# Performance work log

Measured on AMD Instinct MI355X. Metric: run time of the kernel, lower is better.

## Reference

```python
import jax, jax.numpy as jnp
import numpy as np

# Module constants (match init_kwargs / torch defaults)
NUM_HEADS = 8
A, B_COEF, C_COEF = 0.5, 1.0, 1.0
EPS = 1e-12  # torch F.normalize eps


def _l2_normalize(x):
    n = jnp.maximum(jnp.linalg.norm(x, axis=-1, keepdims=True), EPS)
    return x / n


def setup_inputs() -> dict:
    key = jax.random.key(0)
    ks = jax.random.split(key, 4)
    Bb, N, C = 1, 4096, 384
    x = jax.random.normal(ks[0], (Bb, N, C), dtype=jnp.float32)
    qkv_w = jax.random.normal(ks[1], (3 * C, C), dtype=jnp.float32) * 0.02
    qkv_b = jnp.zeros((3 * C,), dtype=jnp.float32)
    proj_w = jax.random.normal(ks[2], (C, C), dtype=jnp.float32) * 0.02
    proj_b = jnp.zeros((C,), dtype=jnp.float32)
    temperature = jnp.ones((1, NUM_HEADS, 1, 1), dtype=jnp.float32)
    return {"x": x, "qkv_w": qkv_w, "qkv_b": qkv_b, "proj_w": proj_w,
            "proj_b": proj_b, "temperature": temperature}


def reference(x, qkv_w, qkv_b, proj_w, proj_b, temperature):
    Bb, N, C = x.shape
    H = NUM_HEADS
    d = C // H
    scale = d ** 0.25

    qkv = x @ qkv_w.T + qkv_b                       # (B, N, 3C)
    qkv = qkv.reshape(Bb, N, 3, H, d).transpose(2, 0, 3, 1, 4)  # (3, B, H, N, d)
    q, k, v = qkv[0], qkv[1], qkv[2]
    q = q * (C ** -0.5)

    # efficient attention (N > N0 = d^2 + d + 1)
    v1 = jnp.concatenate([jnp.ones((Bb, H, N, 1), dtype=v.dtype), v], axis=-1)  # (B,H,N,d+1)
    # normalize_input=True path
    q = _l2_normalize(q) * (scale * temperature)
    k = _l2_normalize(k) * scale
    v1 = v1 / N

    # kv_mod = box(k,k)^T @ v1  ->  (B, H, d, d, d+1)
    kv_mod = jnp.einsum('bhni,bhnj,bhnf->bhijf', k, k, v1)
    # quadratic term: a * box(q,q) @ kv_mod
    y = A * jnp.einsum('bhni,bhnj,bhijf->bhnf', q, q, kv_mod)
    # linear term: scale^2 * b * q @ (k^T @ v1)
    kv = jnp.einsum('bhnd,bhnf->bhdf', k, v1)
    y = y + (scale ** 2) * B_COEF * jnp.einsum('bhnd,bhdf->bhnf', q, kv)
    # constant term: scale^4 * c * sum_n v1
    y = y + (scale ** 4) * C_COEF * jnp.sum(v1, axis=-2, keepdims=True)

    y_norm, y_out = y[..., :1], y[..., 1:]
    out = y_out / y_norm                             # (B, H, N, d)

    out = out.transpose(0, 2, 1, 3).reshape(Bb, N, C)
    out = out @ proj_w.T + proj_b
    return out
```

## Files before the change

kernel.cpp:

```cpp
#include <hip/hip_runtime.h>

#define HN 8
#define NN 4096
#define CC 384
#define DD 48
#define DP 64
#define NPAIR 1225
#define PPAD 1280
#define MPF 52

typedef unsigned short ushort;
typedef unsigned int uint;
typedef __attribute__((ext_vector_type(8))) short short8;
typedef __attribute__((ext_vector_type(4))) float f32x4;

__device__ __forceinline__ float4 ld4(const float* p){ return *reinterpret_cast<const float4*>(p); }
__device__ __forceinline__ void st4(float* p, const float4& v){ *reinterpret_cast<float4*>(p) = v; }

#define RAW_BAR() asm volatile("s_waitcnt lgkmcnt(0)\ns_barrier" ::: "memory")

__device__ __forceinline__ uint bf16rtn(float x){
  uint u = __float_as_uint(x);
  return (u + 0x7FFFu + ((u >> 16) & 1u)) >> 16;
}

__global__ __launch_bounds__(256) void split_f32(const float* __restrict__ in,
                                                 ushort* __restrict__ hi,
                                                 ushort* __restrict__ lo,
                                                 int n4) {
  int idx = blockIdx.x * 256 + threadIdx.x;
  if (idx >= n4) return;
  float4 v = ld4(in + (size_t)idx * 4);
  float bv[4] = {v.x, v.y, v.z, v.w};
  uint hu[2], lu[2];
#pragma unroll
  for (int e = 0; e < 2; ++e) {
    float x0 = bv[2*e], x1 = bv[2*e+1];
    uint h0 = bf16rtn(x0), h1 = bf16rtn(x1);
    float d0 = x0 - __uint_as_float(h0 << 16);
    float d1 = x1 - __uint_as_float(h1 << 16);
    hu[e] = h0 | (h1 << 16);
    lu[e] = (__float_as_uint(d0) >> 16) | (__float_as_uint(d1) & 0xFFFF0000u);
  }
  *reinterpret_cast<uint2*>(hi + (size_t)idx*4) = make_uint2(hu[0], hu[1]);
  *reinterpret_cast<uint2*>(lo + (size_t)idx*4) = make_uint2(lu[0], lu[1]);
}

#define GST 40
__global__ __launch_bounds__(256) void gemm_bf16(const ushort* __restrict__ Ah,
                                                 const ushort* __restrict__ Al,
                                                 const float*  __restrict__ Bw,
                                                 const float*  __restrict__ bias,
                                                 float* __restrict__ Cm,
                                                 int M, int Nc, int K) {
  __shared__ ushort AsH[2][128*GST], AsL[2][128*GST];
  __shared__ ushort BsH[2][64*GST],  BsL[2][64*GST];
  const int tid = threadIdx.x;
  const int n0 = blockIdx.x * 64;
  const int m0 = blockIdx.y * 128;
  const int lane = tid & 63, wv = tid >> 6;
  const int wr = wv >> 1, wc = wv & 1;
  const int lr = lane & 15, lg = lane >> 4;
  const int ar = tid >> 1, ap = (tid & 1) << 4;
  const int br = tid >> 2, bp = (tid & 3) << 3;
  const ushort* gAh = Ah + (size_t)(m0 + ar) * K + ap;
  const ushort* gAl = Al + (size_t)(m0 + ar) * K + ap;
  const float*  gB  = Bw + (size_t)(n0 + br) * K + bp;
  uint4 rah0, rah1, ral0, ral1;
  float4 rb0, rb1;
#define G_LOAD(T) { int kk = (T)*32; \
    rah0 = *reinterpret_cast<const uint4*>(gAh + kk); \
    rah1 = *reinterpret_cast<const uint4*>(gAh + kk + 8); \
    ral0 = *reinterpret_cast<const uint4*>(gAl + kk); \
    ral1 = *reinterpret_cast<const uint4*>(gAl + kk + 8); \
    rb0 = ld4(gB + kk); rb1 = ld4(gB + kk + 4); }
#define G_WRITE(BUF) { \
    *reinterpret_cast<uint4*>(&AsH[BUF][ar*GST+ap])   = rah0; \
    *reinterpret_cast<uint4*>(&AsH[BUF][ar*GST+ap+8]) = rah1; \
    *reinterpret_cast<uint4*>(&AsL[BUF][ar*GST+ap])   = ral0; \
    *reinterpret_cast<uint4*>(&AsL[BUF][ar*GST+ap+8]) = ral1; \
    float bv[8] = {rb0.x,rb0.y,rb0.z,rb0.w,rb1.x,rb1.y,rb1.z,rb1.w}; \
    uint hu[4], lu[4]; \
    _Pragma("unroll") for (int e = 0; e < 4; ++e) { \
      float x0 = bv[2*e], x1 = bv[2*e+1]; \
      uint h0 = bf16rtn(x0), h1 = bf16rtn(x1); \
      float d0 = x0 - __uint_as_float(h0 << 16); \
      float d1 = x1 - __uint_as_float(h1 << 16); \
      hu[e] = h0 | (h1 << 16); \
      lu[e] = (__float_as_uint(d0) >> 16) | (__float_as_uint(d1) & 0xFFFF0000u); } \
    *reinterpret_cast<uint4*>(&BsH[BUF][br*GST+bp]) = make_uint4(hu[0],hu[1],hu[2],hu[3]); \
    *reinterpret_cast<uint4*>(&BsL[BUF][br*GST+bp]) = make_uint4(lu[0],lu[1],lu[2],lu[3]); }

  f32x4 acc[4][2];
#pragma unroll
  for (int pf = 0; pf < 4; ++pf)
#pragma unroll
    for (int ff = 0; ff < 2; ++ff) acc[pf][ff] = (f32x4)0.f;

  G_LOAD(0);
  G_WRITE(0);
  G_LOAD(1);
  const int NT = K / 32;
  int cur = 0;
  RAW_BAR();
  for (int t = 0; t < NT; ++t) {
    short8 a_h[4], a_l[4], b_h[2], b_l[2];
#pragma unroll
    for (int pf = 0; pf < 4; ++pf) {
      int row = wr*64 + pf*16 + lr;
      a_h[pf] = *reinterpret_cast<const short8*>(&AsH[cur][row*GST + lg*8]);
      a_l[pf] = *reinterpret_cast<const short8*>(&AsL[cur][row*GST + lg*8]);
    }
#pragma unroll
    for (int ff = 0; ff < 2; ++ff) {
      int col = wc*32 + ff*16 + lr;
      b_h[ff] = *reinterpret_cast<const short8*>(&BsH[cur][col*GST + lg*8]);
      b_l[ff] = *reinterpret_cast<const short8*>(&BsL[cur][col*GST + lg*8]);
    }
    if (t < NT-1) { G_WRITE(cur^1); }
    if (t < NT-2) { G_LOAD(t+2); }
#pragma unroll
    for (int pf = 0; pf < 4; ++pf)
#pragma unroll
      for (int ff = 0; ff < 2; ++ff) {
        acc[pf][ff] = __builtin_amdgcn_mfma_f32_16x16x32_bf16(a_h[pf], b_h[ff], acc[pf][ff], 0, 0, 0);
        acc[pf][ff] = __builtin_amdgcn_mfma_f32_16x16x32_bf16(a_h[pf], b_l[ff], acc[pf][ff], 0, 0, 0);
        acc[pf][ff] = __builtin_amdgcn_mfma_f32_16x16x32_bf16(a_l[pf], b_h[ff], acc[pf][ff], 0, 0, 0);
      }
    RAW_BAR();
    cur ^= 1;
  }
#pragma unroll
  for (int pf = 0; pf < 4; ++pf)
#pragma unroll
    for (int ff = 0; ff < 2; ++ff) {
      int col = n0 + wc*32 + ff*16 + lr;
      float bs = bias[col];
#pragma unroll
      for (int reg = 0; reg < 4; ++reg) {
        int row = m0 + wr*64 + pf*16 + lg*4 + reg;
        Cm[(size_t)row*Nc + col] = acc[pf][ff][reg] + bs;
      }
    }
#undef G_LOAD
#undef G_WRITE
}

__global__ __launch_bounds__(256) void prep2(const float* __restrict__ qkv,
                                             const float* __restrict__ temperature,
                                             float* __restrict__ Qb,
                                             float* __restrict__ KbT,
                                             ushort* __restrict__ VhT,
                                             ushort* __restrict__ VlT) {
  __shared__ float Ks[64*65];
  __shared__ float Vs[64*65];
  const int nb = blockIdx.x;
  const int h  = blockIdx.y;
  const int lane = threadIdx.x & 63;
  const int w = threadIdx.x >> 6;
  const float temp = temperature[h];
  const float CINV = 0.05103103630798288f;
  const float S4   = 2.6321480259049848f;
  for (int r = 0; r < 16; ++r) {
    const int nl = w*16 + r;
    const int n  = nb*64 + nl;
    const float* row = qkv + (size_t)n * (3*CC) + h * DD;
    float qv = (lane < DD) ? row[lane] : 0.f;
    float kv = (lane < DD) ? row[CC + lane] : 0.f;
    float vv = (lane >= 1 && lane <= DD) ? row[2*CC + lane - 1] : 0.f;
    float qs = qv * CINV;
    float q2 = qs * qs;
    float k2 = kv * kv;
#pragma unroll
    for (int off = 32; off > 0; off >>= 1) {
      q2 += __shfl_xor(q2, off);
      k2 += __shfl_xor(k2, off);
    }
    float qn = qs / fmaxf(sqrtf(q2), 1e-12f) * (S4 * temp);
    float kn = kv / fmaxf(sqrtf(k2), 1e-12f) * S4;
    float qo = (lane < DD) ? qn : ((lane == DD) ? 6.928203230275509f : 0.f);
    float ko = (lane < DD) ? kn : ((lane == DD) ? 1.f : 0.f);
    float vo = (lane == 0) ? (1.f/NN) : ((lane <= DD) ? vv * (1.f/NN) : 0.f);
    Qb[((size_t)h * NN + n) * DP + lane] = qo;
    Ks[nl*65 + lane] = ko;
    Vs[nl*65 + lane] = vo;
  }
  __syncthreads();
  const int ch = threadIdx.x >> 2;
  const int q4 = threadIdx.x & 3;
  float kc[16], vc[16];
#pragma unroll
  for (int e = 0; e < 16; ++e) {
    int nl = q4*16 + e;
    kc[e] = Ks[nl*65 + ch];
    vc[e] = Vs[nl*65 + ch];
  }
  size_t tbase = ((size_t)h*64 + ch) * NN + nb*64 + q4*16;
#pragma unroll
  for (int e = 0; e < 16; e += 4)
    st4(KbT + tbase + e, make_float4(kc[e], kc[e+1], kc[e+2], kc[e+3]));
  uint hu[8], lu[8];
#pragma unroll
  for (int e = 0; e < 8; ++e) {
    float v0 = vc[2*e], v1 = vc[2*e+1];
    uint h0 = bf16rtn(v0), h1 = bf16rtn(v1);
    float d0 = v0 - __uint_as_float(h0 << 16);
    float d1 = v1 - __uint_as_float(h1 << 16);
    uint t0 = __float_as_uint(d0), t1 = __float_as_uint(d1);
    hu[e] = h0 | (h1 << 16);
    lu[e] = (t0 >> 16) | (t1 & 0xFFFF0000u);
  }
  *reinterpret_cast<uint4*>(VhT + tbase)     = make_uint4(hu[0],hu[1],hu[2],hu[3]);
  *reinterpret_cast<uint4*>(VhT + tbase + 8) = make_uint4(hu[4],hu[5],hu[6],hu[7]);
  *reinterpret_cast<uint4*>(VlT + tbase)     = make_uint4(lu[0],lu[1],lu[2],lu[3]);
  *reinterpret_cast<uint4*>(VlT + tbase + 8) = make_uint4(lu[4],lu[5],lu[6],lu[7]);
}

#define KST 40
#define KNST 36
__global__ __launch_bounds__(256) void kvmod_mfma(const float* __restrict__ KbT,
                                                  const ushort* __restrict__ VhT,
                                                  const ushort* __restrict__ VlT,
                                                  float* __restrict__ Mp) {
  __shared__ ushort KKh[256*KST];
  __shared__ ushort KKl[256*KST];
  __shared__ float  KnS[64*KNST];
  __shared__ ushort VhS[64*KST];
  __shared__ ushort VlS[64*KST];
  const int tid  = threadIdx.x;
  const int bid  = blockIdx.x;
  const int h    = bid & 7;
  const int idx  = bid >> 3;
  const int p0   = (idx % 5) * 256;
  const int part = idx / 5;
  const int nbase = part * 512;
  int ii = 63, jj = 63;
  {
    int pg = p0 + tid;
    if (pg < NPAIR) {
      int i = 0, rem = pg;
      while (rem >= 49 - i) { rem -= 49 - i; ++i; }
      ii = i; jj = i + rem;
    }
  }
  const float* krow_i = &KnS[ii*KNST];
  const float* krow_j = &KnS[jj*KNST];
  const int sch = tid >> 2;
  const int sq  = tid & 3;
  const size_t kgbase = ((size_t)h*64 + sch) * NN + nbase;
  const int lane = tid & 63, wv = tid >> 6;
  const int lr = lane & 15, lg = lane >> 4;
  f32x4 acc[4][4];
#pragma unroll
  for (int a = 0; a < 4; ++a)
#pragma unroll
    for (int b = 0; b < 4; ++b) acc[a][b] = (f32x4)0.f;

  float4 pa0, pa1; uint4 pvh, pvl;
#define PRE_LOAD(T) { int k0_ = (T)*32; \
    pa0 = ld4(KbT + kgbase + k0_ + sq*8); \
    pa1 = ld4(KbT + kgbase + k0_ + sq*8 + 4); \
    pvh = *reinterpret_cast<const uint4*>(VhT + kgbase + k0_ + sq*8); \
    pvl = *reinterpret_cast<const uint4*>(VlT + kgbase + k0_ + sq*8); }
#define STAGE_WRITE() { \
    st4(&KnS[sch*KNST + sq*8], pa0); \
    st4(&KnS[sch*KNST + sq*8 + 4], pa1); \
    *reinterpret_cast<uint4*>(&VhS[sch*KST + sq*8]) = pvh; \
    *reinterpret_cast<uint4*>(&VlS[sch*KST + sq*8]) = pvl; }

  PRE_LOAD(0);
  for (int t = 0; t < 16; ++t) {
    RAW_BAR();
    STAGE_WRITE();
    if (t < 15) { PRE_LOAD(t+1); }
    RAW_BAR();
    {
      uint hu[16], lu[16];
#pragma unroll
      for (int g = 0; g < 8; ++g) {
        float4 a = ld4(krow_i + g*4);
        float4 b = ld4(krow_j + g*4);
        float m0 = a.x*b.x, m1 = a.y*b.y, m2 = a.z*b.z, m3 = a.w*b.w;
        uint h0 = bf16rtn(m0), h1 = bf16rtn(m1), h2 = bf16rtn(m2), h3 = bf16rtn(m3);
        float d0 = m0 - __uint_as_float(h0 << 16);
        float d1 = m1 - __uint_as_float(h1 << 16);
        float d2 = m2 - __uint_as_float(h2 << 16);
        float d3 = m3 - __uint_as_float(h3 << 16);
        uint t0 = __float_as_uint(d0), t1 = __float_as_uint(d1);
        uint t2 = __float_as_uint(d2), t3 = __float_as_uint(d3);
        hu[2*g]   = h0 | (h1 << 16);
        hu[2*g+1] = h2 | (h3 << 16);
        lu[2*g]   = (t0 >> 16) | (t1 & 0xFFFF0000u);
        lu[2*g+1] = (t2 >> 16) | (t3 & 0xFFFF0000u);
      }
      uint4* dh = reinterpret_cast<uint4*>(&KKh[tid*KST]);
      uint4* dl = reinterpret_cast<uint4*>(&KKl[tid*KST]);
      dh[0] = make_uint4(hu[0],hu[1],hu[2],hu[3]);
      dh[1] = make_uint4(hu[4],hu[5],hu[6],hu[7]);
      dh[2] = make_uint4(hu[8],hu[9],hu[10],hu[11]);
      dh[3] = make_uint4(hu[12],hu[13],hu[14],hu[15]);
      dl[0] = make_uint4(lu[0],lu[1],lu[2],lu[3]);
      dl[1] = make_uint4(lu[4],lu[5],lu[6],lu[7]);
      dl[2] = make_uint4(lu[8],lu[9],lu[10],lu[11]);
      dl[3] = make_uint4(lu[12],lu[13],lu[14],lu[15]);
    }
    RAW_BAR();
    short8 ah[4], al[4], bh[4], bl[4];
#pragma unroll
    for (int pf = 0; pf < 4; ++pf) {
      int prow = wv*64 + pf*16 + lr;
      ah[pf] = *reinterpret_cast<const short8*>(&KKh[prow*KST + lg*8]);
      al[pf] = *reinterpret_cast<const short8*>(&KKl[prow*KST + lg*8]);
    }
#pragma unroll
    for (int ff = 0; ff < 4; ++ff) {
      int frow = ff*16 + lr;
      bh[ff] = *reinterpret_cast<const short8*>(&VhS[frow*KST + lg*8]);
      bl[ff] = *reinterpret_cast<const short8*>(&VlS[frow*KST + lg*8]);
    }
#pragma unroll
    for (int pf = 0; pf < 4; ++pf)
#pragma unroll
      for (int ff = 0; ff < 4; ++ff) {
        acc[pf][ff] = __builtin_amdgcn_mfma_f32_16x16x32_bf16(ah[pf], bh[ff], acc[pf][ff], 0, 0, 0);
        acc[pf][ff] = __builtin_amdgcn_mfma_f32_16x16x32_bf16(ah[pf], bl[ff], acc[pf][ff], 0, 0, 0);
        acc[pf][ff] = __builtin_amdgcn_mfma_f32_16x16x32_bf16(al[pf], bh[ff], acc[pf][ff], 0, 0, 0);
      }
  }
  float* out = Mp + ((size_t)(part*HN + h) * PPAD + p0 + wv*64) * MPF;
#pragma unroll
  for (int pf = 0; pf < 4; ++pf)
#pragma unroll
    for (int ff = 0; ff < 4; ++ff) {
      int f = ff*16 + lr;
      if (f < MPF) {
#pragma unroll
        for (int reg = 0; reg < 4; ++reg) {
          int prow = pf*16 + lg*4 + reg;
          out[prow*MPF + f] = acc[pf][ff][reg];
        }
      }
    }
#undef PRE_LOAD
#undef STAGE_WRITE
}

__global__ __launch_bounds__(256) void reduce_mirror(const float* __restrict__ Mp,
                                                     ushort* __restrict__ Mbh,
                                                     ushort* __restrict__ Mbl,
                                                     float* __restrict__ Mnorm) {
  const int pb = blockIdx.x;
  const int h  = blockIdx.y;
  const int pl = threadIdx.x & 63;
  const int fq0 = threadIdx.x >> 6;
  const int p = pb*64 + pl;
  if (p >= NPAIR) return;
  int i = 0, rem = p;
  while (rem >= 49 - i) { rem -= 49 - i; ++i; }
  const int j = i + rem;
  for (int fq = fq0; fq < 13; fq += 4) {
    float4 s = make_float4(0.f, 0.f, 0.f, 0.f);
#pragma unroll
    for (int part = 0; part < 8; ++part) {
      float4 a = ld4(Mp + ((size_t)(part*HN + h) * PPAD + p) * MPF + fq*4);
      s.x += a.x; s.y += a.y; s.z += a.z; s.w += a.w;
    }
    float sv[4] = {s.x, s.y, s.z, s.w};
#pragma unroll
    for (int c = 0; c < 4; ++c) {
      int f = fq*4 + c;
      float v = sv[c];
      uint hb = bf16rtn(v);
      float d = v - __uint_as_float(hb << 16);
      ushort lb = (ushort)(__float_as_uint(d) >> 16);
      size_t a1 = (((size_t)h*49 + i)*64 + f)*64 + j;
      size_t a2 = (((size_t)h*49 + j)*64 + f)*64 + i;
      Mbh[a1] = (ushort)hb; Mbl[a1] = lb;
      Mbh[a2] = (ushort)hb; Mbl[a2] = lb;
    }
    if (p == NPAIR-1) st4(&Mnorm[h*64 + fq*4], s);
  }
}

__global__ __launch_bounds__(256, 3) void y_mfma(const float* __restrict__ Qb,
                                                 const ushort* __restrict__ Mbh,
                                                 const ushort* __restrict__ Mbl,
                                                 float* __restrict__ Yp) {
  __shared__ float QT[28*128];
  __shared__ ushort Mt[2][2][32*64];
  const int tid = threadIdx.x;
  const int bid = blockIdx.x;
  const int h   = bid & 7;
  const int rest = bid >> 3;
  const int n0  = (rest & 31) * 128;
  const int z   = rest >> 5;
  const int zi = z >> 1;
  const int zf = z & 1;
  const int ibase = zi * 25;
  const int ni = zi ? 24 : 25;
  const int lane = tid & 63;
  const int wv = tid >> 6;
  const int lr = lane & 15, lg = lane >> 4;

  {
    const int ng = (ni + 3) >> 2;
    for (int v = tid; v < ng*128; v += 256) {
      int r = v & 127;
      int cg = v >> 7;
      float4 q = ld4(Qb + ((size_t)h*NN + n0 + r)*DP + ibase + cg*4);
      QT[(cg*4+0)*128 + r] = q.x;
      QT[(cg*4+1)*128 + r] = q.y;
      QT[(cg*4+2)*128 + r] = q.z;
      QT[(cg*4+3)*128 + r] = q.w;
    }
  }
  short8 ah[2][2], al[2][2];
#pragma unroll
  for (int m = 0; m < 2; ++m) {
    const float* qr = Qb + ((size_t)h*NN + n0 + wv*32 + m*16 + lr)*DP + lg*8;
#pragma unroll
    for (int kc = 0; kc < 2; ++kc) {
      float4 v0 = ld4(qr + kc*32);
      float4 v1 = ld4(qr + kc*32 + 4);
      float qv[8] = {v0.x,v0.y,v0.z,v0.w,v1.x,v1.y,v1.z,v1.w};
      union { uint u[4]; short8 s; } chh, cll;
#pragma unroll
      for (int e = 0; e < 4; ++e) {
        float x0 = qv[2*e], x1 = qv[2*e+1];
        uint h0 = bf16rtn(x0), h1 = bf16rtn(x1);
        float d0 = x0 - __uint_as_float(h0 << 16);
        float d1 = x1 - __uint_as_float(h1 << 16);
        chh.u[e] = h0 | (h1 << 16);
        cll.u[e] = (__float_as_uint(d0) >> 16) | (__float_as_uint(d1) & 0xFFFF0000u);
      }
      ah[m][kc] = chh.s;
      al[m][kc] = cll.s;
    }
  }
  const int sp   = tid >> 7;
  const int ss   = tid & 127;
  const int srow = ss >> 2;
  const int sc2  = (ss & 3) * 2;
  const ushort* gsrc = (sp ? Mbl : Mbh) + (size_t)h*49*4096 + (zf*32 + srow)*64 + sc2*8;
  uint4 pre[2];
#define Y_LOAD(I) { const uint4* gp = reinterpret_cast<const uint4*>(gsrc + (size_t)(I)*4096); \
    pre[0] = gp[0]; pre[1] = gp[1]; }
#define Y_WRITE(BUF) { _Pragma("unroll") for (int e = 0; e < 2; ++e) { \
    int slot = (sc2 + e) ^ (srow & 7); \
    *reinterpret_cast<uint4*>(&Mt[BUF][sp][srow*64 + slot*8]) = pre[e]; } }

  Y_LOAD(ibase);
  Y_WRITE(0);
  Y_LOAD(ibase+1);

  f32x4 ya[2][2];
#pragma unroll
  for (int m = 0; m < 2; ++m)
#pragma unroll
    for (int ff = 0; ff < 2; ++ff) ya[m][ff] = (f32x4)0.f;

  int cur = 0;
  RAW_BAR();
  for (int li = 0; li < ni; ++li) {
    short8 bh[2][2], bl[2][2];
#pragma unroll
    for (int kc = 0; kc < 2; ++kc)
#pragma unroll
      for (int ff = 0; ff < 2; ++ff) {
        int row = ff*16 + lr;
        int slot = (kc*4 + lg) ^ (row & 7);
        bh[kc][ff] = *reinterpret_cast<const short8*>(&Mt[cur][0][row*64 + slot*8]);
        bl[kc][ff] = *reinterpret_cast<const short8*>(&Mt[cur][1][row*64 + slot*8]);
      }
    if (li < ni-1) { Y_WRITE(cur^1); }
    if (li < ni-2) { Y_LOAD(ibase+li+2); }
#pragma unroll
    for (int m = 0; m < 2; ++m) {
      float4 qi = ld4(&QT[li*128 + wv*32 + m*16 + lg*4]);
#pragma unroll
      for (int ff = 0; ff < 2; ++ff) {
        f32x4 acc = (f32x4)0.f;
        acc = __builtin_amdgcn_mfma_f32_16x16x32_bf16(ah[m][0], bh[0][ff], acc, 0, 0, 0);
        acc = __builtin_amdgcn_mfma_f32_16x16x32_bf16(ah[m][0], bl[0][ff], acc, 0, 0, 0);
        acc = __builtin_amdgcn_mfma_f32_16x16x32_bf16(al[m][0], bh[0][ff], acc, 0, 0, 0);
        acc = __builtin_amdgcn_mfma_f32_16x16x32_bf16(ah[m][1], bh[1][ff], acc, 0, 0, 0);
        acc = __builtin_amdgcn_mfma_f32_16x16x32_bf16(ah[m][1], bl[1][ff], acc, 0, 0, 0);
        acc = __builtin_amdgcn_mfma_f32_16x16x32_bf16(al[m][1], bh[1][ff], acc, 0, 0, 0);
        ya[m][ff][0] += qi.x * acc[0];
        ya[m][ff][1] += qi.y * acc[1];
        ya[m][ff][2] += qi.z * acc[2];
        ya[m][ff][3] += qi.w * acc[3];
      }
    }
    RAW_BAR();
    cur ^= 1;
  }
  float* out = Yp + ((size_t)(zi*HN + h) * NN) * 64;
#pragma unroll
  for (int m = 0; m < 2; ++m)
#pragma unroll
    for (int ff = 0; ff < 2; ++ff) {
      int f = zf*32 + ff*16 + lr;
#pragma unroll
      for (int reg = 0; reg < 4; ++reg) {
        int row = n0 + wv*32 + m*16 + lg*4 + reg;
        out[(size_t)row*64 + f] = ya[m][ff][reg];
      }
    }
#undef Y_LOAD
#undef Y_WRITE
}

__global__ __launch_bounds__(256) void y_combine(const float* __restrict__ Yp,
                                                 const float* __restrict__ Mnorm,
                                                 ushort* __restrict__ AttnH,
                                                 ushort* __restrict__ AttnL) {
  const int h = blockIdx.y;
  const int t = threadIdx.x;
  const int r = blockIdx.x*64 + (t >> 2);
  const int fq = t & 3;
  const int lane = t & 63;
  const float* p0 = Yp + ((size_t)h*NN + r)*64 + fq*16;
  const float* p1 = Yp + ((size_t)(HN+h)*NN + r)*64 + fq*16;
  float y[16];
#pragma unroll
  for (int g = 0; g < 4; ++g) {
    float4 a = ld4(p0 + g*4);
    float4 b = ld4(p1 + g*4);
    float4 m = ld4(Mnorm + h*64 + fq*16 + g*4);
    y[g*4+0] = 0.5f*(a.x+b.x) + 24.f*m.x;
    y[g*4+1] = 0.5f*(a.y+b.y) + 24.f*m.y;
    y[g*4+2] = 0.5f*(a.z+b.z) + 24.f*m.z;
    y[g*4+3] = 0.5f*(a.w+b.w) + 24.f*m.w;
  }
  float y0 = __shfl(y[0], lane & ~3);
  float inv = 1.f / y0;
#pragma unroll
  for (int e = 0; e < 16; ++e) {
    int f = fq*16 + e;
    if (f >= 1 && f <= DD) {
      float o = y[e] * inv;
      uint hb = bf16rtn(o);
      float d = o - __uint_as_float(hb << 16);
      size_t a = (size_t)r*CC + h*DD + (f-1);
      AttnH[a] = (ushort)hb;
      AttnL[a] = (ushort)(__float_as_uint(d) >> 16);
    }
  }
}

extern "C" void kernel_launch(void* const* d_in, const int* in_sizes, int n_in,
                              void* d_out, int out_size, void* d_ws, size_t ws_size,
                              hipStream_t stream) {
  const float* x      = (const float*)d_in[0];
  const float* qkv_w  = (const float*)d_in[1];
  const float* qkv_b  = (const float*)d_in[2];
  const float* proj_w = (const float*)d_in[3];
  const float* proj_b = (const float*)d_in[4];
  const float* temp   = (const float*)d_in[5];
  float* ws = (float*)d_ws;

  float*  qkv  = ws;
  float*  Mp   = ws;
  float*  Yp   = ws;
  float*  Qb   = ws + 4718592;
  ushort* Xh   = (ushort*)(ws + 6815744);
  ushort* Xl   = Xh + 1572864;
  float*  KbT  = ws + 6815744;
  ushort* Mbh  = (ushort*)(ws + 6815744);
  ushort* Mbl  = Mbh + 1605632;
  float*  Mnorm= ws + 6815744 + 1605632;
  ushort* VhT  = (ushort*)(ws + 8912896);
  ushort* VlT  = (ushort*)(ws + 9961472);
  ushort* AttnH= (ushort*)(ws + 8912896);
  ushort* AttnL= AttnH + 1572864;

  split_f32<<<1536, 256, 0, stream>>>(x, Xh, Xl, NN*CC/4);
  {
    dim3 g(1152/64, 4096/128);
    gemm_bf16<<<g, 256, 0, stream>>>(Xh, Xl, qkv_w, qkv_b, qkv, 4096, 1152, 384);
  }
  {
    dim3 g(64, HN);
    prep2<<<g, 256, 0, stream>>>(qkv, temp, Qb, KbT, VhT, VlT);
  }
  kvmod_mfma<<<320, 256, 0, stream>>>(KbT, VhT, VlT, Mp);
  hipMemsetAsync((void*)Mbh, 0, 2*(size_t)1605632*2 + 2048, stream);
  {
    dim3 g(PPAD/64, HN);
    reduce_mirror<<<g, 256, 0, stream>>>(Mp, Mbh, Mbl, Mnorm);
  }
  y_mfma<<<1024, 256, 0, stream>>>(Qb, Mbh, Mbl, Yp);
  {
    dim3 g(4096/64, HN);
    y_combine<<<g, 256, 0, stream>>>(Yp, Mnorm, AttnH, AttnL);
  }
  {
    dim3 g(384/64, 4096/128);
    gemm_bf16<<<g, 256, 0, stream>>>(AttnH, AttnL, proj_w, proj_b, (float*)d_out, 4096, 384, 384);
  }
}
```

Before: 201.4 us.

## Exploit pair symmetry in quadratic attention term with packed upper-triangle layout

Instead of mirroring the symmetric kv_mod tensor to a full 49x49 layout and contracting q with it in two stages, the reduction now stores only upper-triangle pairs (diagonal halved) in a chunked, transposed layout. The y kernel builds q_i*q_j products on the fly and feeds them as the MFMA A operand over the packed pair dimension. This roughly halves the K dimension and the M tensor traffic, and drops the 0.5 factor in the combine step to match. The cost is recomputing pair products and the bf16 hi/lo split per tile, plus a more intricate chunk index mapping.

```diff
diff --git a/kernel.cpp b/kernel.cpp
--- a/kernel.cpp
+++ b/kernel.cpp
@@ -8,6 +8,8 @@
 #define NPAIR 1225
 #define PPAD 1280
 #define MPF 52
+#define NP2 1792
+#define QRS 68
 
 typedef unsigned short ushort;
 typedef unsigned int uint;
@@ -22,6 +24,16 @@
 __device__ __forceinline__ uint bf16rtn(float x){
   uint u = __float_as_uint(x);
   return (u + 0x7FFFu + ((u >> 16) & 1u)) >> 16;
+}
+
+__device__ __forceinline__ void chunk_ij(int c, int& i, int& jb){
+  if (c < 56)       { i = c/7;            jb = c%7; }
+  else if (c < 104) { int t=c-56;  i = 8  + t/6; jb = 1 + t%6; }
+  else if (c < 144) { int t=c-104; i = 16 + t/5; jb = 2 + t%5; }
+  else if (c < 176) { int t=c-144; i = 24 + t/4; jb = 3 + t%4; }
+  else if (c < 200) { int t=c-176; i = 32 + t/3; jb = 4 + t%3; }
+  else if (c < 216) { int t=c-200; i = 40 + t/2; jb = 5 + t%2; }
+  else              { i = 48 + (c-216);   jb = 6; }
 }
 
 __global__ __launch_bounds__(256) void split_f32(const float* __restrict__ in,
@@ -345,170 +357,142 @@
 #undef STAGE_WRITE
 }
 
-__global__ __launch_bounds__(256) void reduce_mirror(const float* __restrict__ Mp,
-                                                     ushort* __restrict__ Mbh,
-                                                     ushort* __restrict__ Mbl,
-                                                     float* __restrict__ Mnorm) {
+__global__ __launch_bounds__(256) void reduce_pair(const float* __restrict__ Mp,
+                                                   ushort* __restrict__ MpTh,
+                                                   ushort* __restrict__ MpTl,
+                                                   float* __restrict__ Mnorm) {
   const int pb = blockIdx.x;
   const int h  = blockIdx.y;
   const int pl = threadIdx.x & 63;
   const int fq0 = threadIdx.x >> 6;
   const int p = pb*64 + pl;
-  if (p >= NPAIR) return;
-  int i = 0, rem = p;
-  while (rem >= 49 - i) { rem -= 49 - i; ++i; }
-  const int j = i + rem;
+  const int c = p >> 3, e = p & 7;
+  int ci, cjb;
+  chunk_ij(c, ci, cjb);
+  const int j = cjb*8 + e;
+  if (ci > 48 || j < ci || j > 48) return;
+  const int oldp = ci*49 - (ci*(ci-1))/2 + (j - ci);
+  const float scale = (ci == j) ? 0.5f : 1.0f;
+  const bool isnorm = (ci == 48) && (j == 48);
   for (int fq = fq0; fq < 13; fq += 4) {
     float4 s = make_float4(0.f, 0.f, 0.f, 0.f);
 #pragma unroll
     for (int part = 0; part < 8; ++part) {
-      float4 a = ld4(Mp + ((size_t)(part*HN + h) * PPAD + p) * MPF + fq*4);
+      float4 a = ld4(Mp + ((size_t)(part*HN + h) * PPAD + oldp) * MPF + fq*4);
       s.x += a.x; s.y += a.y; s.z += a.z; s.w += a.w;
     }
-    float sv[4] = {s.x, s.y, s.z, s.w};
-#pragma unroll
-    for (int c = 0; c < 4; ++c) {
-      int f = fq*4 + c;
-      float v = sv[c];
+    if (isnorm) st4(&Mnorm[h*64 + fq*4], s);
+    float sv[4] = {s.x*scale, s.y*scale, s.z*scale, s.w*scale};
+#pragma unroll
+    for (int c4 = 0; c4 < 4; ++c4) {
+      int f = fq*4 + c4;
+      float v = sv[c4];
       uint hb = bf16rtn(v);
       float d = v - __uint_as_float(hb << 16);
-      ushort lb = (ushort)(__float_as_uint(d) >> 16);
-      size_t a1 = (((size_t)h*49 + i)*64 + f)*64 + j;
-      size_t a2 = (((size_t)h*49 + j)*64 + f)*64 + i;
-      Mbh[a1] = (ushort)hb; Mbl[a1] = lb;
-      Mbh[a2] = (ushort)hb; Mbl[a2] = lb;
-    }
-    if (p == NPAIR-1) st4(&Mnorm[h*64 + fq*4], s);
-  }
-}
-
-__global__ __launch_bounds__(256, 3) void y_mfma(const float* __restrict__ Qb,
-                                                 const ushort* __restrict__ Mbh,
-                                                 const ushort* __restrict__ Mbl,
+      size_t a = ((size_t)h*64 + f) * NP2 + p;
+      MpTh[a] = (ushort)hb;
+      MpTl[a] = (ushort)(__float_as_uint(d) >> 16);
+    }
+  }
+}
+
+__global__ __launch_bounds__(256, 3) void y_pair(const float* __restrict__ Qb,
+                                                 const ushort* __restrict__ MpTh,
+                                                 const ushort* __restrict__ MpTl,
                                                  float* __restrict__ Yp) {
-  __shared__ float QT[28*128];
-  __shared__ ushort Mt[2][2][32*64];
+  __shared__ float Qrow[128*QRS];
+  __shared__ ushort Bt[2][64*40];
   const int tid = threadIdx.x;
   const int bid = blockIdx.x;
   const int h   = bid & 7;
-  const int rest = bid >> 3;
-  const int n0  = (rest & 31) * 128;
-  const int z   = rest >> 5;
-  const int zi = z >> 1;
-  const int zf = z & 1;
-  const int ibase = zi * 25;
-  const int ni = zi ? 24 : 25;
-  const int lane = tid & 63;
-  const int wv = tid >> 6;
+  const int nt  = (bid >> 3) & 31;
+  const int zk  = bid >> 8;
+  const int n0  = nt * 128;
+  const int lane = tid & 63, wv = tid >> 6;
+  const int wr = wv >> 1, wc = wv & 1;
   const int lr = lane & 15, lg = lane >> 4;
 
-  {
-    const int ng = (ni + 3) >> 2;
-    for (int v = tid; v < ng*128; v += 256) {
-      int r = v & 127;
-      int cg = v >> 7;
-      float4 q = ld4(Qb + ((size_t)h*NN + n0 + r)*DP + ibase + cg*4);
-      QT[(cg*4+0)*128 + r] = q.x;
-      QT[(cg*4+1)*128 + r] = q.y;
-      QT[(cg*4+2)*128 + r] = q.z;
-      QT[(cg*4+3)*128 + r] = q.w;
-    }
-  }
-  short8 ah[2][2], al[2][2];
-#pragma unroll
-  for (int m = 0; m < 2; ++m) {
-    const float* qr = Qb + ((size_t)h*NN + n0 + wv*32 + m*16 + lr)*DP + lg*8;
-#pragma unroll
-    for (int kc = 0; kc < 2; ++kc) {
-      float4 v0 = ld4(qr + kc*32);
-      float4 v1 = ld4(qr + kc*32 + 4);
-      float qv[8] = {v0.x,v0.y,v0.z,v0.w,v1.x,v1.y,v1.z,v1.w};
-      union { uint u[4]; short8 s; } chh, cll;
-#pragma unroll
-      for (int e = 0; e < 4; ++e) {
-        float x0 = qv[2*e], x1 = qv[2*e+1];
+  for (int v = tid; v < 128*16; v += 256) {
+    int r = v >> 4, cg = v & 15;
+    float4 q = ld4(Qb + ((size_t)h*NN + n0 + r)*DP + cg*4);
+    float* d = &Qrow[r*QRS + cg*4];
+    d[0]=q.x; d[1]=q.y; d[2]=q.z; d[3]=q.w;
+  }
+  const int sp = tid >> 7;
+  const int sidx = tid & 127;
+  const int sf = sidx >> 1;
+  const int sph = (sidx & 1) * 16;
+  const ushort* gB = (sp ? MpTl : MpTh) + ((size_t)h*64 + sf)*NP2 + zk*896 + sph;
+  uint4 pb0, pb1;
+#define B_LOAD(T) { const uint4* gp = reinterpret_cast<const uint4*>(gB + (size_t)(T)*32); \
+    pb0 = gp[0]; pb1 = gp[1]; }
+#define B_WRITE() { \
+    *reinterpret_cast<uint4*>(&Bt[sp][sf*40 + sph])     = pb0; \
+    *reinterpret_cast<uint4*>(&Bt[sp][sf*40 + sph + 8]) = pb1; }
+
+  f32x4 acc[4][2];
+#pragma unroll
+  for (int m = 0; m < 4; ++m)
+#pragma unroll
+    for (int ff = 0; ff < 2; ++ff) acc[m][ff] = (f32x4)0.f;
+
+  B_LOAD(0);
+  RAW_BAR();
+  for (int t = 0; t < 28; ++t) {
+    B_WRITE();
+    if (t < 27) { B_LOAD(t+1); }
+    int c = (zk*28 + t)*4 + lg;
+    int ci, cjb;
+    chunk_ij(c, ci, cjb);
+    RAW_BAR();
+    short8 bfh[2], bfl[2];
+#pragma unroll
+    for (int ff = 0; ff < 2; ++ff) {
+      int f = wc*32 + ff*16 + lr;
+      bfh[ff] = *reinterpret_cast<const short8*>(&Bt[0][f*40 + lg*8]);
+      bfl[ff] = *reinterpret_cast<const short8*>(&Bt[1][f*40 + lg*8]);
+    }
+#pragma unroll
+    for (int m = 0; m < 4; ++m) {
+      int row = wr*64 + m*16 + lr;
+      float qi = Qrow[row*QRS + ci];
+      float4 qa = ld4(&Qrow[row*QRS + cjb*8]);
+      float4 qb = ld4(&Qrow[row*QRS + cjb*8 + 4]);
+      float xs[8] = {qi*qa.x, qi*qa.y, qi*qa.z, qi*qa.w,
+                     qi*qb.x, qi*qb.y, qi*qb.z, qi*qb.w};
+      union { uint u[4]; short8 s; } uh, ul;
+#pragma unroll
+      for (int e2 = 0; e2 < 4; ++e2) {
+        float x0 = xs[2*e2], x1 = xs[2*e2+1];
         uint h0 = bf16rtn(x0), h1 = bf16rtn(x1);
         float d0 = x0 - __uint_as_float(h0 << 16);
         float d1 = x1 - __uint_as_float(h1 << 16);
-        chh.u[e] = h0 | (h1 << 16);
-        cll.u[e] = (__float_as_uint(d0) >> 16) | (__float_as_uint(d1) & 0xFFFF0000u);
-      }
-      ah[m][kc] = chh.s;
-      al[m][kc] = cll.s;
-    }
-  }
-  const int sp   = tid >> 7;
-  const int ss   = tid & 127;
-  const int srow = ss >> 2;
-  const int sc2  = (ss & 3) * 2;
-  const ushort* gsrc = (sp ? Mbl : Mbh) + (size_t)h*49*4096 + (zf*32 + srow)*64 + sc2*8;
-  uint4 pre[2];
-#define Y_LOAD(I) { const uint4* gp = reinterpret_cast<const uint4*>(gsrc + (size_t)(I)*4096); \
-    pre[0] = gp[0]; pre[1] = gp[1]; }
-#define Y_WRITE(BUF) { _Pragma("unroll") for (int e = 0; e < 2; ++e) { \
-    int slot = (sc2 + e) ^ (srow & 7); \
-    *reinterpret_cast<uint4*>(&Mt[BUF][sp][srow*64 + slot*8]) = pre[e]; } }
-
-  Y_LOAD(ibase);
-  Y_WRITE(0);
-  Y_LOAD(ibase+1);
-
-  f32x4 ya[2][2];
-#pragma unroll
-  for (int m = 0; m < 2; ++m)
-#pragma unroll
-    for (int ff = 0; ff < 2; ++ff) ya[m][ff] = (f32x4)0.f;
-
-  int cur = 0;
-  RAW_BAR();
-  for (int li = 0; li < ni; ++li) {
-    short8 bh[2][2], bl[2][2];
-#pragma unroll
-    for (int kc = 0; kc < 2; ++kc)
+        uh.u[e2] = h0 | (h1 << 16);
+        ul.u[e2] = (__float_as_uint(d0) >> 16) | (__float_as_uint(d1) & 0xFFFF0000u);
+      }
 #pragma unroll
       for (int ff = 0; ff < 2; ++ff) {
-        int row = ff*16 + lr;
-        int slot = (kc*4 + lg) ^ (row & 7);
-        bh[kc][ff] = *reinterpret_cast<const short8*>(&Mt[cur][0][row*64 + slot*8]);
-        bl[kc][ff] = *reinterpret_cast<const short8*>(&Mt[cur][1][row*64 + slot*8]);
-      }
-    if (li < ni-1) { Y_WRITE(cur^1); }
-    if (li < ni-2) { Y_LOAD(ibase+li+2); }
-#pragma unroll
-    for (int m = 0; m < 2; ++m) {
-      float4 qi = ld4(&QT[li*128 + wv*32 + m*16 + lg*4]);
-#pragma unroll
-      for (int ff = 0; ff < 2; ++ff) {
-        f32x4 acc = (f32x4)0.f;
-        acc = __builtin_amdgcn_mfma_f32_16x16x32_bf16(ah[m][0], bh[0][ff], acc, 0, 0, 0);
-        acc = __builtin_amdgcn_mfma_f32_16x16x32_bf16(ah[m][0], bl[0][ff], acc, 0, 0, 0);
-        acc = __builtin_amdgcn_mfma_f32_16x16x32_bf16(al[m][0], bh[0][ff], acc, 0, 0, 0);
-        acc = __builtin_amdgcn_mfma_f32_16x16x32_bf16(ah[m][1], bh[1][ff], acc, 0, 0, 0);
-        acc = __builtin_amdgcn_mfma_f32_16x16x32_bf16(ah[m][1], bl[1][ff], acc, 0, 0, 0);
-        acc = __builtin_amdgcn_mfma_f32_16x16x32_bf16(al[m][1], bh[1][ff], acc, 0, 0, 0);
-        ya[m][ff][0] += qi.x * acc[0];
-        ya[m][ff][1] += qi.y * acc[1];
-        ya[m][ff][2] += qi.z * acc[2];
-        ya[m][ff][3] += qi.w * acc[3];
+        acc[m][ff] = __builtin_amdgcn_mfma_f32_16x16x32_bf16(uh.s, bfh[ff], acc[m][ff], 0, 0, 0);
+        acc[m][ff] = __builtin_amdgcn_mfma_f32_16x16x32_bf16(uh.s, bfl[ff], acc[m][ff], 0, 0, 0);
+        acc[m][ff] = __builtin_amdgcn_mfma_f32_16x16x32_bf16(ul.s, bfh[ff], acc[m][ff], 0, 0, 0);
       }
     }
     RAW_BAR();
-    cur ^= 1;
-  }
-  float* out = Yp + ((size_t)(zi*HN + h) * NN) * 64;
-#pragma unroll
-  for (int m = 0; m < 2; ++m)
+  }
+  float* out = Yp + ((size_t)(zk*HN + h) * NN) * 64;
+#pragma unroll
+  for (int m = 0; m < 4; ++m)
 #pragma unroll
     for (int ff = 0; ff < 2; ++ff) {
-      int f = zf*32 + ff*16 + lr;
+      int f = wc*32 + ff*16 + lr;
 #pragma unroll
       for (int reg = 0; reg < 4; ++reg) {
-        int row = n0 + wv*32 + m*16 + lg*4 + reg;
-        out[(size_t)row*64 + f] = ya[m][ff][reg];
-      }
-    }
-#undef Y_LOAD
-#undef Y_WRITE
+        int row = n0 + wr*64 + m*16 + lg*4 + reg;
+        out[(size_t)row*64 + f] = acc[m][ff][reg];
+      }
+    }
+#undef B_LOAD
+#undef B_WRITE
 }
 
 __global__ __launch_bounds__(256) void y_combine(const float* __restrict__ Yp,
@@ -528,10 +512,10 @@
     float4 a = ld4(p0 + g*4);
     float4 b = ld4(p1 + g*4);
     float4 m = ld4(Mnorm + h*64 + fq*16 + g*4);
-    y[g*4+0] = 0.5f*(a.x+b.x) + 24.f*m.x;
-    y[g*4+1] = 0.5f*(a.y+b.y) + 24.f*m.y;
-    y[g*4+2] = 0.5f*(a.z+b.z) + 24.f*m.z;
-    y[g*4+3] = 0.5f*(a.w+b.w) + 24.f*m.w;
+    y[g*4+0] = (a.x+b.x) + 24.f*m.x;
+    y[g*4+1] = (a.y+b.y) + 24.f*m.y;
+    y[g*4+2] = (a.z+b.z) + 24.f*m.z;
+    y[g*4+3] = (a.w+b.w) + 24.f*m.w;
   }
   float y0 = __shfl(y[0], lane & ~3);
   float inv = 1.f / y0;
@@ -567,9 +551,9 @@
   ushort* Xh   = (ushort*)(ws + 6815744);
   ushort* Xl   = Xh + 1572864;
   float*  KbT  = ws + 6815744;
-  ushort* Mbh  = (ushort*)(ws + 6815744);
-  ushort* Mbl  = Mbh + 1605632;
-  float*  Mnorm= ws + 6815744 + 1605632;
+  ushort* MpTh = (ushort*)(ws + 6815744);
+  ushort* MpTl = MpTh + 917504;
+  float*  Mnorm= ws + 6815744 + 917504;
   ushort* VhT  = (ushort*)(ws + 8912896);
   ushort* VlT  = (ushort*)(ws + 9961472);
   ushort* AttnH= (ushort*)(ws + 8912896);
@@ -585,12 +569,12 @@
     prep2<<<g, 256, 0, stream>>>(qkv, temp, Qb, KbT, VhT, VlT);
   }
   kvmod_mfma<<<320, 256, 0, stream>>>(KbT, VhT, VlT, Mp);
-  hipMemsetAsync((void*)Mbh, 0, 2*(size_t)1605632*2 + 2048, stream);
+  hipMemsetAsync((void*)MpTh, 0, (size_t)917504*2*2 + 2048, stream);
   {
-    dim3 g(PPAD/64, HN);
-    reduce_mirror<<<g, 256, 0, stream>>>(Mp, Mbh, Mbl, Mnorm);
-  }
-  y_mfma<<<1024, 256, 0, stream>>>(Qb, Mbh, Mbl, Yp);
+    dim3 g(NP2/64, HN);
+    reduce_pair<<<g, 256, 0, stream>>>(Mp, MpTh, MpTl, Mnorm);
+  }
+  y_pair<<<512, 256, 0, stream>>>(Qb, MpTh, MpTl, Yp);
   {
     dim3 g(4096/64, HN);
     y_combine<<<g, 256, 0, stream>>>(Yp, Mnorm, AttnH, AttnL);
```

Measured after the change: 178.5 us (median of 3 runs). -11.4%, faster.
